# Optimization experiments

Measured on AMD Instinct MI355X. Metric: run time of the kernel, lower is better.

## Reference

```python
import jax, jax.numpy as jnp
import numpy as np

N = 50000        # nodes
E = 800000       # edges (avg degree 16)
IN = 256         # in_feature
HID = 32         # hidden per head
HEADS = 4        # gat_heads
OUT = 64         # out_feature
SLOPE = 0.2      # PyG GATConv default negative_slope


def _gat_layer(x, src, dst, edge_weight, W, a_src, a_dst, b, heads, ch, concat):
    """One GATConv: linear -> per-edge attention logits -> segment softmax over
    incoming edges of each dst node -> weighted scatter-sum. edge_weight scales
    the unnormalized attention (log-space edge weighting, identity at init=1)."""
    n = x.shape[0]
    h = (x @ W).reshape(n, heads, ch)                       # [N,H,C]
    al_s = jnp.einsum('nhc,hc->nh', h, a_src)               # [N,H]
    al_d = jnp.einsum('nhc,hc->nh', h, a_dst)               # [N,H]
    logit = jax.nn.leaky_relu(al_s[src] + al_d[dst], SLOPE) # [E,H]
    m = jax.lax.stop_gradient(jax.ops.segment_max(logit, dst, num_segments=n))
    e = jnp.exp(logit - m[dst]) * edge_weight[:, None]      # [E,H]
    denom = jax.ops.segment_sum(e, dst, num_segments=n)     # [N,H]
    alpha = e / (denom[dst] + 1e-16)                        # [E,H]
    out = jax.ops.segment_sum(h[src] * alpha[..., None], dst, num_segments=n)
    out = out.reshape(n, heads * ch) if concat else out.mean(axis=1)
    return out + b


def setup_inputs() -> dict:
    key = jax.random.key(0)
    ks = jax.random.split(key, 14)
    s = 0.1
    x = jax.random.normal(ks[0], (N, IN), jnp.float32)
    edge_index = jax.random.randint(ks[1], (2, E), 0, N, dtype=jnp.int64)
    edge_weight = jnp.ones((E,), jnp.float32)
    D1 = HEADS * HID
    W1 = jax.random.normal(ks[2], (IN, D1), jnp.float32) * s
    a_src1 = jax.random.normal(ks[3], (HEADS, HID), jnp.float32) * s
    a_dst1 = jax.random.normal(ks[4], (HEADS, HID), jnp.float32) * s
    b1 = jnp.zeros((D1,), jnp.float32)
    W2 = jax.random.normal(ks[5], (D1, D1), jnp.float32) * s
    a_src2 = jax.random.normal(ks[6], (HEADS, HID), jnp.float32) * s
    a_dst2 = jax.random.normal(ks[7], (HEADS, HID), jnp.float32) * s
    b2 = jnp.zeros((D1,), jnp.float32)
    W3 = jax.random.normal(ks[8], (D1, OUT), jnp.float32) * s
    a_src3 = jax.random.normal(ks[9], (1, OUT), jnp.float32) * s
    a_dst3 = jax.random.normal(ks[10], (1, OUT), jnp.float32) * s
    b3 = jnp.zeros((OUT,), jnp.float32)
    return dict(x=x, edge_index=edge_index, edge_weight=edge_weight,
                W1=W1, a_src1=a_src1, a_dst1=a_dst1, b1=b1,
                W2=W2, a_src2=a_src2, a_dst2=a_dst2, b2=b2,
                W3=W3, a_src3=a_src3, a_dst3=a_dst3, b3=b3)


def reference(x, edge_index, edge_weight,
              W1, a_src1, a_dst1, b1,
              W2, a_src2, a_dst2, b2,
              W3, a_src3, a_dst3, b3):
    src, dst = edge_index[0], edge_index[1]
    h = _gat_layer(x, src, dst, edge_weight, W1, a_src1, a_dst1, b1, HEADS, HID, True)
    h = jax.nn.relu(h)  # dropout = identity in eval mode
    h = _gat_layer(h, src, dst, edge_weight, W2, a_src2, a_dst2, b2, HEADS, HID, True)
    h = jax.nn.relu(h)
    out = _gat_layer(h, src, dst, edge_weight, W3, a_src3, a_dst3, b3, 1, OUT, False)
    return out
```

## Files before the change

kernel.cpp:

```cpp
#include <hip/hip_runtime.h>
#include <math.h>

#define NNODES 50000
#define NEDGES 800000

#define BIN_SHIFT 9
#define BIN_W 512
#define NBINS 98
#define CAP 12288
#define ATILE 4096

typedef _Float16 f16;
typedef __attribute__((ext_vector_type(2))) _Float16 f16x2;
typedef __attribute__((ext_vector_type(4))) _Float16 f16x4;
typedef __attribute__((ext_vector_type(8))) _Float16 f16x8;
typedef __attribute__((ext_vector_type(4))) float f32x4;

__device__ __forceinline__ float leaky02(float v) { return v > 0.f ? v : 0.2f * v; }


__global__ __launch_bounds__(256) void init_kernel(int* __restrict__ binCursor,
                                                   const float* __restrict__ W1,
                                                   const float* __restrict__ W2,
                                                   const float* __restrict__ W3,
                                                   f16* __restrict__ WT1,
                                                   f16* __restrict__ WT2,
                                                   f16* __restrict__ WT3) {
  int gid = blockIdx.x * 256 + threadIdx.x;
  int stride = gridDim.x * 256;
  if (gid < NBINS) binCursor[gid] = 0;
  for (int i = gid; i < 32768; i += stride) {
    int d = i >> 8, k = i & 255;
    WT1[i] = (f16)W1[k * 128 + d];
  }
  for (int i = gid; i < 16384; i += stride) {
    int d = i >> 7, k = i & 127;
    WT2[i] = (f16)W2[k * 128 + d];
  }
  for (int i = gid; i < 8192; i += stride) {
    int d = i >> 7, k = i & 127;
    WT3[i] = (f16)W3[k * 64 + d];
  }
}


__global__ __launch_bounds__(256) void bin_kernel(const int* __restrict__ dst,
                                                  const int* __restrict__ src,
                                                  const float* __restrict__ ew,
                                                  int* __restrict__ binCursor,
                                                  int2* __restrict__ binned, int ne) {
  __shared__ int cnt[NBINS];
  __shared__ int gbase[NBINS];
  int tid = threadIdx.x;
  int t0 = blockIdx.x * ATILE;
  if (tid < NBINS) cnt[tid] = 0;
  __syncthreads();
  int saved[ATILE / 256];
  #pragma unroll
  for (int u = 0; u < ATILE / 256; ++u) {
    int i = t0 + u * 256 + tid;
    int v = 0;
    if (i < ne) {
      int d = dst[i];
      int idx = atomicAdd(&cnt[d >> BIN_SHIFT], 1);
      v = d | (idx << 16);
    }
    saved[u] = v;
  }
  __syncthreads();
  if (tid < NBINS) gbase[tid] = atomicAdd(&binCursor[tid], cnt[tid]);
  __syncthreads();
  #pragma unroll
  for (int u = 0; u < ATILE / 256; ++u) {
    int i = t0 + u * 256 + tid;
    if (i < ne) {
      int v = saved[u];
      int d = v & 0xffff;
      int idx = (int)((unsigned)v >> 16);
      int b = d >> BIN_SHIFT;
      int slot = gbase[b] + idx;
      if (slot < CAP)
        binned[(size_t)b * CAP + slot] =
            make_int2(src[i] | (d << 16), __float_as_int(ew[i]));
    }
  }
}


__global__ __launch_bounds__(256) void build_kernel(const int2* __restrict__ binned,
                                                    const int* __restrict__ binCursor,
                                                    int* __restrict__ offsets,
                                                    int2* __restrict__ edgeSW, int n) {
  __shared__ int sizes[NBINS];
  __shared__ int cnt[BIN_W];
  __shared__ int wsum[4];
  __shared__ int bstartS;
  int tid = threadIdx.x;
  int b = blockIdx.x;
  if (tid < NBINS) sizes[tid] = binCursor[tid];
  cnt[tid] = 0;
  cnt[tid + 256] = 0;
  __syncthreads();
  if (tid == 0) {
    int s = 0;
    for (int k = 0; k < b; ++k) s += (sizes[k] < CAP ? sizes[k] : CAP);
    bstartS = s;
  }
  int mySize = sizes[b];
  if (mySize > CAP) mySize = CAP;
  __syncthreads();
  const int2* mybin = binned + (size_t)b * CAP;
  for (int i = tid; i < mySize; i += 256)
    atomicAdd(&cnt[((unsigned)mybin[i].x >> 16) - b * BIN_W], 1);
  __syncthreads();
  int c0 = cnt[2 * tid], c1 = cnt[2 * tid + 1];
  int s2 = c0 + c1;
  int lane = tid & 63, wid = tid >> 6;
  int incl = s2;
  #pragma unroll
  for (int o = 1; o < 64; o <<= 1) {
    int u = __shfl_up(incl, o, 64);
    if (lane >= o) incl += u;
  }
  if (lane == 63) wsum[wid] = incl;
  __syncthreads();
  if (tid == 0) {
    int r = 0;
    #pragma unroll
    for (int w = 0; w < 4; ++w) { int t = wsum[w]; wsum[w] = r; r += t; }
  }
  __syncthreads();
  int excl0 = bstartS + wsum[wid] + incl - s2;
  int excl1 = excl0 + c0;
  int node0 = b * BIN_W;
  if (node0 + 2 * tid < n)     offsets[node0 + 2 * tid]     = excl0;
  if (node0 + 2 * tid + 1 < n) offsets[node0 + 2 * tid + 1] = excl1;
  if (b == NBINS - 1 && tid == 0) offsets[n] = bstartS + mySize;
  __syncthreads();
  cnt[2 * tid] = excl0;
  cnt[2 * tid + 1] = excl1;
  __syncthreads();
  for (int i = tid; i < mySize; i += 256) {
    int2 r = mybin[i];
    int dloc = (int)((unsigned)r.x >> 16) - b * BIN_W;
    int pos = atomicAdd(&cnt[dloc], 1);
    edgeSW[pos] = make_int2(r.x & 0xffff, r.y);
  }
}


template<typename AT, int BN, int H>
__global__ __launch_bounds__(256) void gemm_mfma_kernel(const AT* __restrict__ A,
                                                        const f16* __restrict__ BT,
                                                        f16* __restrict__ C,
                                                        const float* __restrict__ a_src,
                                                        const float* __restrict__ a_dst,
                                                        float* __restrict__ als,
                                                        float* __restrict__ ald,
                                                        int M, int K) {
  constexpr int BM = 64;
  constexpr int WN = BN / 2;
  constexpr int MT = 2, NT = WN / 16;
  __shared__ f16 As[BM * 72];
  __shared__ f16 Bs[BN * 72];
  __shared__ float redS[2][2][32], redD[2][2][32];
  int tid = threadIdx.x;
  int lane = tid & 63, wave = tid >> 6;
  int wm = wave & 1, wn = wave >> 1;
  int row0 = blockIdx.x * BM;
  int quad = lane >> 4, cc = lane & 15;

  f32x4 acc[MT][NT];
  #pragma unroll
  for (int mt = 0; mt < MT; ++mt)
    #pragma unroll
    for (int nt = 0; nt < NT; ++nt)
      acc[mt][nt] = (f32x4){0.f, 0.f, 0.f, 0.f};

  for (int k0 = 0; k0 < K; k0 += 64) {
    __syncthreads();
    if constexpr (sizeof(AT) == 4) {
      #pragma unroll
      for (int i = 0; i < 4; ++i) {
        int r = i * 16 + (tid >> 4);
        int kc = (tid & 15) * 4;
        float4 av = make_float4(0.f, 0.f, 0.f, 0.f);
        if (row0 + r < M) av = *(const float4*)&A[(size_t)(row0 + r) * K + k0 + kc];
        *(f16x4*)&As[r * 72 + kc] = (f16x4){(f16)av.x, (f16)av.y, (f16)av.z, (f16)av.w};
      }
    } else {
      #pragma unroll
      for (int i = 0; i < 2; ++i) {
        int r = i * 32 + (tid >> 3);
        int kc = (tid & 7) * 8;
        f16x8 hv = {0, 0, 0, 0, 0, 0, 0, 0};
        if (row0 + r < M) hv = *(const f16x8*)&A[(size_t)(row0 + r) * K + k0 + kc];
        *(f16x8*)&As[r * 72 + kc] = hv;
      }
    }
    #pragma unroll
    for (int i = 0; i < BN / 32; ++i) {
      int d = i * 32 + (tid >> 3);
      int kc = (tid & 7) * 8;
      *(f16x8*)&Bs[d * 72 + kc] = *(const f16x8*)&BT[(size_t)d * K + k0 + kc];
    }
    __syncthreads();
    #pragma unroll
    for (int ki = 0; ki < 2; ++ki) {
      f16x8 a[MT], b[NT];
      #pragma unroll
      for (int mt = 0; mt < MT; ++mt)
        a[mt] = *(const f16x8*)&As[(wm * 32 + mt * 16 + cc) * 72 + ki * 32 + quad * 8];
      #pragma unroll
      for (int nt = 0; nt < NT; ++nt)
        b[nt] = *(const f16x8*)&Bs[(wn * WN + nt * 16 + cc) * 72 + ki * 32 + quad * 8];
      #pragma unroll
      for (int mt = 0; mt < MT; ++mt)
        #pragma unroll
        for (int nt = 0; nt < NT; ++nt)
          acc[mt][nt] = __builtin_amdgcn_mfma_f32_16x16x32_f16(a[mt], b[nt], acc[mt][nt], 0, 0, 0);
    }
  }

  float asv[NT], adv[NT];
  #pragma unroll
  for (int nt = 0; nt < NT; ++nt) {
    int ch = wn * WN + nt * 16 + cc;
    asv[nt] = a_src[ch];
    adv[nt] = a_dst[ch];
  }

  #pragma unroll
  for (int mt = 0; mt < MT; ++mt)
    #pragma unroll
    for (int v = 0; v < 4; ++v) {
      int row = row0 + wm * 32 + mt * 16 + quad * 4 + v;
      if (row < M) {
        #pragma unroll
        for (int nt = 0; nt < NT; ++nt)
          C[(size_t)row * BN + wn * WN + nt * 16 + cc] = (f16)acc[mt][nt][v];
      }
      if constexpr (H == 4) {
        float s0 = acc[mt][0][v] * asv[0] + acc[mt][1][v] * asv[1];
        float s1 = acc[mt][2][v] * asv[2] + acc[mt][3][v] * asv[3];
        float d0 = acc[mt][0][v] * adv[0] + acc[mt][1][v] * adv[1];
        float d1 = acc[mt][2][v] * adv[2] + acc[mt][3][v] * adv[3];
        #pragma unroll
        for (int o = 1; o < 16; o <<= 1) {
          s0 += __shfl_xor(s0, o);
          s1 += __shfl_xor(s1, o);
          d0 += __shfl_xor(d0, o);
          d1 += __shfl_xor(d1, o);
        }
        if (cc == 0 && row < M) {
          *(float2*)&als[row * 4 + 2 * wn] = make_float2(s0, s1);
          *(float2*)&ald[row * 4 + 2 * wn] = make_float2(d0, d1);
        }
      } else {
        float s0 = acc[mt][0][v] * asv[0] + acc[mt][1][v] * asv[1];
        float d0 = acc[mt][0][v] * adv[0] + acc[mt][1][v] * adv[1];
        #pragma unroll
        for (int o = 1; o < 16; o <<= 1) {
          s0 += __shfl_xor(s0, o);
          d0 += __shfl_xor(d0, o);
        }
        int r = mt * 16 + quad * 4 + v;
        if (cc == 0) { redS[wm][wn][r] = s0; redD[wm][wn][r] = d0; }
      }
    }
  if constexpr (H == 1) {
    __syncthreads();
    #pragma unroll
    for (int mt = 0; mt < MT; ++mt)
      #pragma unroll
      for (int v = 0; v < 4; ++v) {
        int row = row0 + wm * 32 + mt * 16 + quad * 4 + v;
        int r = mt * 16 + quad * 4 + v;
        if (wn == 0 && cc == 0 && row < M) {
          als[row] = redS[wm][0][r] + redS[wm][1][r];
          ald[row] = redD[wm][0][r] + redD[wm][1][r];
        }
      }
  }
}


template<bool RELU>
__global__ __launch_bounds__(256) void aggregate4_kernel(const f16* __restrict__ h16,
                                                         const float* __restrict__ als,
                                                         const float* __restrict__ ald,
                                                         const int* __restrict__ offsets,
                                                         const int2* __restrict__ edgeSW,
                                                         const float* __restrict__ bias,
                                                         f16* __restrict__ out, int n_nodes) {
  __shared__ int   swS[8][32];
  __shared__ float swW[8][4][32];
  int hw = threadIdx.x >> 5;
  int hl = threadIdx.x & 31;
  int node = blockIdx.x * 8 + hw;
  bool valid = node < n_nodes;
  int nodeC = valid ? node : n_nodes - 1;
  int start = offsets[nodeC], end = offsets[nodeC + 1];
  int deg = valid ? end - start : 0;

  float4 aldv = *(const float4*)&ald[nodeC * 4];

  int s0 = 0; float wgt0 = 0.f;
  float v0 = 0.f, v1 = 0.f, v2 = 0.f, v3 = 0.f;
  float m0 = -INFINITY, m1 = -INFINITY, m2 = -INFINITY, m3 = -INFINITY;
  if (hl < deg) {
    int2 e = edgeSW[start + hl];
    s0 = e.x;
    wgt0 = __int_as_float(e.y);
    float4 a4 = *(const float4*)&als[s0 * 4];
    v0 = leaky02(a4.x + aldv.x); m0 = v0;
    v1 = leaky02(a4.y + aldv.y); m1 = v1;
    v2 = leaky02(a4.z + aldv.z); m2 = v2;
    v3 = leaky02(a4.w + aldv.w); m3 = v3;
  }
  for (int j = start + 32 + hl; j < end; j += 32) {
    int2 e = edgeSW[j];
    float4 a4 = *(const float4*)&als[e.x * 4];
    m0 = fmaxf(m0, leaky02(a4.x + aldv.x));
    m1 = fmaxf(m1, leaky02(a4.y + aldv.y));
    m2 = fmaxf(m2, leaky02(a4.z + aldv.z));
    m3 = fmaxf(m3, leaky02(a4.w + aldv.w));
  }
  #pragma unroll
  for (int o = 16; o > 0; o >>= 1) {
    m0 = fmaxf(m0, __shfl_xor(m0, o, 32));
    m1 = fmaxf(m1, __shfl_xor(m1, o, 32));
    m2 = fmaxf(m2, __shfl_xor(m2, o, 32));
    m3 = fmaxf(m3, __shfl_xor(m3, o, 32));
  }
  float w0 = 0.f, w1 = 0.f, w2 = 0.f, w3 = 0.f;
  if (hl < deg) {
    w0 = __expf(v0 - m0) * wgt0;
    w1 = __expf(v1 - m1) * wgt0;
    w2 = __expf(v2 - m2) * wgt0;
    w3 = __expf(v3 - m3) * wgt0;
  }
  swS[hw][hl] = s0;
  swW[hw][0][hl] = w0;
  swW[hw][1][hl] = w1;
  swW[hw][2][hl] = w2;
  swW[hw][3][hl] = w3;
  __syncthreads();

  int h2 = hl >> 4, l16 = hl & 15;
  int head = l16 >> 2;
  float acc0 = 0.f, acc1 = 0.f, acc2 = 0.f, acc3 = 0.f;
  float acc4 = 0.f, acc5 = 0.f, acc6 = 0.f, acc7 = 0.f;
  float dd = 0.f;
  int cn = deg < 32 ? deg : 32;
  int nb = (cn + 15) >> 4;
  for (int b = 0; b < nb; ++b) {
    int j0 = b * 16 + h2 * 8;
    int4   sa = *(const int4*)&swS[hw][j0];
    int4   sb = *(const int4*)&swS[hw][j0 + 4];
    float4 wa = *(const float4*)&swW[hw][head][j0];
    float4 wb = *(const float4*)&swW[hw][head][j0 + 4];
    int   sj[8] = {sa.x, sa.y, sa.z, sa.w, sb.x, sb.y, sb.z, sb.w};
    float wj[8] = {wa.x, wa.y, wa.z, wa.w, wb.x, wb.y, wb.z, wb.w};
    f16x8 hv[8];
    #pragma unroll
    for (int u = 0; u < 8; ++u)
      hv[u] = *(const f16x8*)&h16[(size_t)sj[u] * 128 + 8 * l16];
    #pragma unroll
    for (int u = 0; u < 8; ++u) {
      dd += wj[u];
      acc0 += wj[u] * (float)hv[u][0];
      acc1 += wj[u] * (float)hv[u][1];
      acc2 += wj[u] * (float)hv[u][2];
      acc3 += wj[u] * (float)hv[u][3];
      acc4 += wj[u] * (float)hv[u][4];
      acc5 += wj[u] * (float)hv[u][5];
      acc6 += wj[u] * (float)hv[u][6];
      acc7 += wj[u] * (float)hv[u][7];
    }
  }
  for (int base = start + 32; base < end; base += 32) {
    int cnt = end - base; if (cnt > 32) cnt = 32;
    int st = 0; float u0 = 0.f, u1 = 0.f, u2 = 0.f, u3 = 0.f;
    if (hl < cnt) {
      int2 e = edgeSW[base + hl];
      st = e.x;
      float wg = __int_as_float(e.y);
      float4 a4 = *(const float4*)&als[st * 4];
      u0 = __expf(leaky02(a4.x + aldv.x) - m0) * wg;
      u1 = __expf(leaky02(a4.y + aldv.y) - m1) * wg;
      u2 = __expf(leaky02(a4.z + aldv.z) - m2) * wg;
      u3 = __expf(leaky02(a4.w + aldv.w) - m3) * wg;
    }
    for (int jj = h2; jj < cnt; jj += 2) {
      int sjr = __shfl(st, jj, 32);
      float t0 = __shfl(u0, jj, 32), t1 = __shfl(u1, jj, 32);
      float t2 = __shfl(u2, jj, 32), t3 = __shfl(u3, jj, 32);
      float wr = head == 0 ? t0 : head == 1 ? t1 : head == 2 ? t2 : t3;
      f16x8 hv = *(const f16x8*)&h16[(size_t)sjr * 128 + 8 * l16];
      dd += wr;
      acc0 += wr * (float)hv[0];
      acc1 += wr * (float)hv[1];
      acc2 += wr * (float)hv[2];
      acc3 += wr * (float)hv[3];
      acc4 += wr * (float)hv[4];
      acc5 += wr * (float)hv[5];
      acc6 += wr * (float)hv[6];
      acc7 += wr * (float)hv[7];
    }
  }

  acc0 += __shfl_xor(acc0, 16, 32);
  acc1 += __shfl_xor(acc1, 16, 32);
  acc2 += __shfl_xor(acc2, 16, 32);
  acc3 += __shfl_xor(acc3, 16, 32);
  acc4 += __shfl_xor(acc4, 16, 32);
  acc5 += __shfl_xor(acc5, 16, 32);
  acc6 += __shfl_xor(acc6, 16, 32);
  acc7 += __shfl_xor(acc7, 16, 32);
  dd   += __shfl_xor(dd, 16, 32);

  if (valid && h2 == 0) {
    float inv = 1.f / (dd + 1e-16f);
    float4 bv0 = *(const float4*)&bias[8 * l16];
    float4 bv1 = *(const float4*)&bias[8 * l16 + 4];
    float o0 = acc0 * inv + bv0.x, o1 = acc1 * inv + bv0.y;
    float o2 = acc2 * inv + bv0.z, o3 = acc3 * inv + bv0.w;
    float o4 = acc4 * inv + bv1.x, o5 = acc5 * inv + bv1.y;
    float o6 = acc6 * inv + bv1.z, o7 = acc7 * inv + bv1.w;
    if (RELU) {
      o0 = fmaxf(o0, 0.f); o1 = fmaxf(o1, 0.f);
      o2 = fmaxf(o2, 0.f); o3 = fmaxf(o3, 0.f);
      o4 = fmaxf(o4, 0.f); o5 = fmaxf(o5, 0.f);
      o6 = fmaxf(o6, 0.f); o7 = fmaxf(o7, 0.f);
    }
    *(f16x8*)&out[(size_t)node * 128 + 8 * l16] =
        (f16x8){(f16)o0, (f16)o1, (f16)o2, (f16)o3, (f16)o4, (f16)o5, (f16)o6, (f16)o7};
  }
}

__global__ __launch_bounds__(256) void aggregate1_kernel(const f16* __restrict__ h16,
                                                         const float* __restrict__ als,
                                                         const float* __restrict__ ald,
                                                         const int* __restrict__ offsets,
                                                         const int2* __restrict__ edgeSW,
                                                         const float* __restrict__ bias,
                                                         float* __restrict__ out, int n_nodes) {
  __shared__ int   s1s[8][32];
  __shared__ float w1s[8][32];
  int hw = threadIdx.x >> 5;
  int hl = threadIdx.x & 31;
  int node = blockIdx.x * 8 + hw;
  bool valid = node < n_nodes;
  int nodeC = valid ? node : n_nodes - 1;
  int start = offsets[nodeC], end = offsets[nodeC + 1];
  int deg = valid ? end - start : 0;

  float ald0 = ald[nodeC];
  int s0 = 0; float wgt0 = 0.f, v0 = 0.f, m0 = -INFINITY;
  if (hl < deg) {
    int2 e = edgeSW[start + hl];
    s0 = e.x;
    wgt0 = __int_as_float(e.y);
    v0 = leaky02(als[s0] + ald0);
    m0 = v0;
  }
  for (int j = start + 32 + hl; j < end; j += 32) {
    int2 e = edgeSW[j];
    m0 = fmaxf(m0, leaky02(als[e.x] + ald0));
  }
  #pragma unroll
  for (int o = 16; o > 0; o >>= 1) m0 = fmaxf(m0, __shfl_xor(m0, o, 32));

  float w0 = (hl < deg) ? __expf(v0 - m0) * wgt0 : 0.f;
  s1s[hw][hl] = s0;
  w1s[hw][hl] = w0;
  __syncthreads();

  int h2 = hl >> 4, l16 = hl & 15;
  float aX = 0.f, aY = 0.f, aZ = 0.f, aW = 0.f, dd = 0.f;
  int cn = deg < 32 ? deg : 32;
  int nb = (cn + 15) >> 4;
  for (int b = 0; b < nb; ++b) {
    int j0 = b * 16 + h2 * 8;
    int4   sa = *(const int4*)&s1s[hw][j0];
    int4   sb = *(const int4*)&s1s[hw][j0 + 4];
    float4 wa = *(const float4*)&w1s[hw][j0];
    float4 wb = *(const float4*)&w1s[hw][j0 + 4];
    int   sj[8] = {sa.x, sa.y, sa.z, sa.w, sb.x, sb.y, sb.z, sb.w};
    float wj[8] = {wa.x, wa.y, wa.z, wa.w, wb.x, wb.y, wb.z, wb.w};
    f16x4 hv[8];
    #pragma unroll
    for (int u = 0; u < 8; ++u)
      hv[u] = *(const f16x4*)&h16[(size_t)sj[u] * 64 + 4 * l16];
    #pragma unroll
    for (int u = 0; u < 8; ++u) {
      dd += wj[u];
      aX += wj[u] * (float)hv[u][0];
      aY += wj[u] * (float)hv[u][1];
      aZ += wj[u] * (float)hv[u][2];
      aW += wj[u] * (float)hv[u][3];
    }
  }
  for (int base = start + 32; base < end; base += 32) {
    int cnt = end - base; if (cnt > 32) cnt = 32;
    int st = 0; float u0 = 0.f;
    if (hl < cnt) {
      int2 e = edgeSW[base + hl];
      st = e.x;
      u0 = __expf(leaky02(als[st] + ald0) - m0) * __int_as_float(e.y);
    }
    for (int jj = h2; jj < cnt; jj += 2) {
      int sjr = __shfl(st, jj, 32);
      float wr = __shfl(u0, jj, 32);
      f16x4 hv = *(const f16x4*)&h16[(size_t)sjr * 64 + 4 * l16];
      dd += wr;
      aX += wr * (float)hv[0];
      aY += wr * (float)hv[1];
      aZ += wr * (float)hv[2];
      aW += wr * (float)hv[3];
    }
  }

  aX += __shfl_xor(aX, 16, 32);
  aY += __shfl_xor(aY, 16, 32);
  aZ += __shfl_xor(aZ, 16, 32);
  aW += __shfl_xor(aW, 16, 32);
  dd += __shfl_xor(dd, 16, 32);

  if (valid && h2 == 0) {
    float inv = 1.f / (dd + 1e-16f);
    float4 bv = *(const float4*)&bias[4 * l16];
    float4 ov = make_float4(aX * inv + bv.x, aY * inv + bv.y,
                            aZ * inv + bv.z, aW * inv + bv.w);
    *(float4*)&out[(size_t)node * 64 + 4 * l16] = ov;
  }
}


extern "C" void kernel_launch(void* const* d_in, const int* in_sizes, int n_in,
                              void* d_out, int out_size, void* d_ws, size_t ws_size,
                              hipStream_t stream) {
  const int N = NNODES, E = NEDGES;
  const float* x   = (const float*)d_in[0];
  const int*   ei  = (const int*)d_in[1];
  const float* ew  = (const float*)d_in[2];
  const float* W1  = (const float*)d_in[3];
  const float* as1 = (const float*)d_in[4];
  const float* ad1 = (const float*)d_in[5];
  const float* b1  = (const float*)d_in[6];
  const float* W2  = (const float*)d_in[7];
  const float* as2 = (const float*)d_in[8];
  const float* ad2 = (const float*)d_in[9];
  const float* b2  = (const float*)d_in[10];
  const float* W3  = (const float*)d_in[11];
  const float* as3 = (const float*)d_in[12];
  const float* ad3 = (const float*)d_in[13];
  const float* b3  = (const float*)d_in[14];
  const int* src = ei;
  const int* dst = ei + E;

  uint8_t* p = (uint8_t*)d_ws;
  auto carve = [&](size_t bytes) {
    void* r = (void*)p;
    p += (bytes + 255) & ~(size_t)255;
    return r;
  };
  int*   binCursor = (int*)carve((size_t)NBINS * 4);
  int*   offsets   = (int*)carve((size_t)(N + 1) * 4);
  int2*  binned    = (int2*)carve((size_t)NBINS * CAP * 8);
  int2*  edgeSW    = (int2*)carve((size_t)E * 8);
  float* als1      = (float*)carve((size_t)N * 4 * 4);
  float* ald1      = (float*)carve((size_t)N * 4 * 4);
  float* als2      = (float*)carve((size_t)N * 4 * 4);
  float* ald2      = (float*)carve((size_t)N * 4 * 4);
  float* als3      = (float*)carve((size_t)N * 4);
  float* ald3      = (float*)carve((size_t)N * 4);
  f16*   hA16      = (f16*)carve((size_t)N * 128 * 2);
  f16*   hB16      = (f16*)carve((size_t)N * 128 * 2);
  f16*   hC16      = (f16*)carve((size_t)N * 64 * 2);
  f16*   WT1       = (f16*)carve((size_t)256 * 128 * 2);
  f16*   WT2       = (f16*)carve((size_t)128 * 128 * 2);
  f16*   WT3       = (f16*)carve((size_t)128 * 64 * 2);

  init_kernel<<<128, 256, 0, stream>>>(binCursor, W1, W2, W3, WT1, WT2, WT3);
  bin_kernel<<<(E + ATILE - 1) / ATILE, 256, 0, stream>>>(dst, src, ew, binCursor, binned, E);
  build_kernel<<<NBINS, 256, 0, stream>>>(binned, binCursor, offsets, edgeSW, N);

  int gemmGrid = (N + 63) / 64;
  int aggGrid = (N + 7) / 8;

  gemm_mfma_kernel<float, 128, 4><<<gemmGrid, 256, 0, stream>>>(x, WT1, hA16, as1, ad1,
                                                                als1, ald1, N, 256);
  aggregate4_kernel<true><<<aggGrid, 256, 0, stream>>>(hA16, als1, ald1, offsets, edgeSW,
                                                       b1, hB16, N);
  gemm_mfma_kernel<f16, 128, 4><<<gemmGrid, 256, 0, stream>>>(hB16, WT2, hA16, as2, ad2,
                                                              als2, ald2, N, 128);
  aggregate4_kernel<true><<<aggGrid, 256, 0, stream>>>(hA16, als2, ald2, offsets, edgeSW,
                                                       b2, hB16, N);
  gemm_mfma_kernel<f16, 64, 1><<<gemmGrid, 256, 0, stream>>>(hB16, WT3, hC16, as3, ad3,
                                                             als3, ald3, N, 128);
  aggregate1_kernel<<<aggGrid, 256, 0, stream>>>(hC16, als3, ald3, offsets, edgeSW,
                                                 b3, (float*)d_out, N);
}
```

Baseline: 286.8 us.

## Fuse edge binning with first-layer GEMM and use wave-local LDS fences in aggregation

Merges the edge-binning pass and the layer-1 GEMM into a single launch, where block ranges pick which body to run, so the two independent phases overlap and one launch is removed. In the aggregation kernels, the block-wide __syncthreads after writing per-half-wave LDS scratch becomes an lgkmcnt wait, because each 32-lane group only reads its own rows. It also pads the swW shared array to reduce bank conflicts. The risk is that a waitcnt alone is not a full barrier: correctness relies on the half-wave groups sitting inside one wave, and the fused kernel's LDS footprint is the union of both bodies, which may lower occupancy.

```diff
diff --git a/kernel.cpp b/kernel.cpp
--- a/kernel.cpp
+++ b/kernel.cpp
@@ -9,6 +9,7 @@
 #define NBINS 98
 #define CAP 12288
 #define ATILE 4096
+#define NBINBLK ((NEDGES + ATILE - 1) / ATILE)
 
 typedef _Float16 f16;
 typedef __attribute__((ext_vector_type(2))) _Float16 f16x2;
@@ -17,6 +18,10 @@
 typedef __attribute__((ext_vector_type(4))) float f32x4;
 
 __device__ __forceinline__ float leaky02(float v) { return v > 0.f ? v : 0.2f * v; }
+
+__device__ __forceinline__ void wave_lds_fence() {
+  __asm__ volatile("s_waitcnt lgkmcnt(0)" ::: "memory");
+}
 
 
 __global__ __launch_bounds__(256) void init_kernel(int* __restrict__ binCursor,
@@ -44,15 +49,16 @@
 }
 
 
-__global__ __launch_bounds__(256) void bin_kernel(const int* __restrict__ dst,
-                                                  const int* __restrict__ src,
-                                                  const float* __restrict__ ew,
-                                                  int* __restrict__ binCursor,
-                                                  int2* __restrict__ binned, int ne) {
+__device__ __forceinline__ void bin_body(int bid,
+                                         const int* __restrict__ dst,
+                                         const int* __restrict__ src,
+                                         const float* __restrict__ ew,
+                                         int* __restrict__ binCursor,
+                                         int2* __restrict__ binned, int ne) {
   __shared__ int cnt[NBINS];
   __shared__ int gbase[NBINS];
   int tid = threadIdx.x;
-  int t0 = blockIdx.x * ATILE;
+  int t0 = bid * ATILE;
   if (tid < NBINS) cnt[tid] = 0;
   __syncthreads();
   int saved[ATILE / 256];
@@ -150,14 +156,15 @@
 
 
 template<typename AT, int BN, int H>
-__global__ __launch_bounds__(256) void gemm_mfma_kernel(const AT* __restrict__ A,
-                                                        const f16* __restrict__ BT,
-                                                        f16* __restrict__ C,
-                                                        const float* __restrict__ a_src,
-                                                        const float* __restrict__ a_dst,
-                                                        float* __restrict__ als,
-                                                        float* __restrict__ ald,
-                                                        int M, int K) {
+__device__ __forceinline__ void gemm_body(int bid,
+                                          const AT* __restrict__ A,
+                                          const f16* __restrict__ BT,
+                                          f16* __restrict__ C,
+                                          const float* __restrict__ a_src,
+                                          const float* __restrict__ a_dst,
+                                          float* __restrict__ als,
+                                          float* __restrict__ ald,
+                                          int M, int K) {
   constexpr int BM = 64;
   constexpr int WN = BN / 2;
   constexpr int MT = 2, NT = WN / 16;
@@ -167,7 +174,7 @@
   int tid = threadIdx.x;
   int lane = tid & 63, wave = tid >> 6;
   int wm = wave & 1, wn = wave >> 1;
-  int row0 = blockIdx.x * BM;
+  int row0 = bid * BM;
   int quad = lane >> 4, cc = lane & 15;
 
   f32x4 acc[MT][NT];
@@ -284,6 +291,38 @@
   }
 }
 
+template<typename AT, int BN, int H>
+__global__ __launch_bounds__(256) void gemm_mfma_kernel(const AT* __restrict__ A,
+                                                        const f16* __restrict__ BT,
+                                                        f16* __restrict__ C,
+                                                        const float* __restrict__ a_src,
+                                                        const float* __restrict__ a_dst,
+                                                        float* __restrict__ als,
+                                                        float* __restrict__ ald,
+                                                        int M, int K) {
+  gemm_body<AT, BN, H>(blockIdx.x, A, BT, C, a_src, a_dst, als, ald, M, K);
+}
+
+
+__global__ __launch_bounds__(256) void fused_front_kernel(const int* __restrict__ dst,
+                                                          const int* __restrict__ src,
+                                                          const float* __restrict__ ew,
+                                                          int* __restrict__ binCursor,
+                                                          int2* __restrict__ binned, int ne,
+                                                          const float* __restrict__ A,
+                                                          const f16* __restrict__ BT,
+                                                          f16* __restrict__ C,
+                                                          const float* __restrict__ a_src,
+                                                          const float* __restrict__ a_dst,
+                                                          float* __restrict__ als,
+                                                          float* __restrict__ ald,
+                                                          int M, int K) {
+  if (blockIdx.x < NBINBLK)
+    bin_body(blockIdx.x, dst, src, ew, binCursor, binned, ne);
+  else
+    gemm_body<float, 128, 4>(blockIdx.x - NBINBLK, A, BT, C, a_src, a_dst, als, ald, M, K);
+}
+
 
 template<bool RELU>
 __global__ __launch_bounds__(256) void aggregate4_kernel(const f16* __restrict__ h16,
@@ -294,7 +333,7 @@
                                                          const float* __restrict__ bias,
                                                          f16* __restrict__ out, int n_nodes) {
   __shared__ int   swS[8][32];
-  __shared__ float swW[8][4][32];
+  __shared__ float swW[8][4][36];
   int hw = threadIdx.x >> 5;
   int hl = threadIdx.x & 31;
   int node = blockIdx.x * 8 + hw;
@@ -345,7 +384,7 @@
   swW[hw][1][hl] = w1;
   swW[hw][2][hl] = w2;
   swW[hw][3][hl] = w3;
-  __syncthreads();
+  wave_lds_fence();
 
   int h2 = hl >> 4, l16 = hl & 15;
   int head = l16 >> 2;
@@ -475,7 +514,7 @@
   float w0 = (hl < deg) ? __expf(v0 - m0) * wgt0 : 0.f;
   s1s[hw][hl] = s0;
   w1s[hw][hl] = w0;
-  __syncthreads();
+  wave_lds_fence();
 
   int h2 = hl >> 4, l16 = hl & 15;
   float aX = 0.f, aY = 0.f, aZ = 0.f, aW = 0.f, dd = 0.f;
@@ -583,15 +622,16 @@
   f16*   WT2       = (f16*)carve((size_t)128 * 128 * 2);
   f16*   WT3       = (f16*)carve((size_t)128 * 64 * 2);
 
-  init_kernel<<<128, 256, 0, stream>>>(binCursor, W1, W2, W3, WT1, WT2, WT3);
-  bin_kernel<<<(E + ATILE - 1) / ATILE, 256, 0, stream>>>(dst, src, ew, binCursor, binned, E);
-  build_kernel<<<NBINS, 256, 0, stream>>>(binned, binCursor, offsets, edgeSW, N);
-
   int gemmGrid = (N + 63) / 64;
   int aggGrid = (N + 7) / 8;
 
-  gemm_mfma_kernel<float, 128, 4><<<gemmGrid, 256, 0, stream>>>(x, WT1, hA16, as1, ad1,
-                                                                als1, ald1, N, 256);
+  init_kernel<<<128, 256, 0, stream>>>(binCursor, W1, W2, W3, WT1, WT2, WT3);
+
+  fused_front_kernel<<<NBINBLK + gemmGrid, 256, 0, stream>>>(
+      dst, src, ew, binCursor, binned, E,
+      x, WT1, hA16, as1, ad1, als1, ald1, N, 256);
+  build_kernel<<<NBINS, 256, 0, stream>>>(binned, binCursor, offsets, edgeSW, N);
+
   aggregate4_kernel<true><<<aggGrid, 256, 0, stream>>>(hA16, als1, ald1, offsets, edgeSW,
                                                        b1, hB16, N);
   gemm_mfma_kernel<f16, 128, 4><<<gemmGrid, 256, 0, stream>>>(hB16, WT2, hA16, as2, ad2,
```

New measurement: 270.8 us. 5.6% less time.
